# Kernel tuning notes

Hardware: AMD Instinct MI355X
Metric: run time of the kernel (lower is better)

Reference implementation:

```python
import jax, jax.numpy as jnp
import numpy as np

N_NODES = 10000
N_EDGES = 160000
NF = 512  # node_features
DIMS = [1, 2 * NF // 8, 4 * NF // 8, NF]  # 1 -> 128 -> 256 -> 512


def setup_inputs() -> dict:
    key = jax.random.key(0)
    ks = jax.random.split(key, 10)
    inp = {
        "x": jax.random.normal(ks[0], (N_NODES, 1), dtype=jnp.float32),
        "edge_index": jax.random.randint(ks[1], (2, N_EDGES), 0, N_NODES, dtype=jnp.int64),
        "edge_weights": jax.random.uniform(ks[2], (N_EDGES,), dtype=jnp.float32),
    }
    # Glorot-style init for GCNConv linear weights, zero biases (PyG default)
    for i in range(3):
        d_in, d_out = DIMS[i], DIMS[i + 1]
        scale = (6.0 / (d_in + d_out)) ** 0.5
        inp[f"W{i+1}"] = jax.random.uniform(ks[3 + i], (d_in, d_out), dtype=jnp.float32, minval=-scale, maxval=scale)
        inp[f"b{i+1}"] = jnp.zeros((d_out,), dtype=jnp.float32)
    return inp


def _gcn_layer(h, W, b, src, dst, ew):
    # GCNConv with add_self_loops=False, normalize=False:
    #   h' = scatter_sum(edge_weight * (h @ W)[src] -> dst) + b
    h = h @ W                                    # [N, d_out]
    msg = h[src] * ew[:, None]                   # [E, d_out] gather + scale
    agg = jax.ops.segment_sum(msg, dst, num_segments=N_NODES)  # scatter-add
    return agg + b


def reference(x, edge_index, edge_weights, W1, b1, W2, b2, W3, b3):
    src, dst = edge_index[0], edge_index[1]  # source_to_target flow
    h = _gcn_layer(x, W1, b1, src, dst, edge_weights)
    h = _gcn_layer(h, W2, b2, src, dst, edge_weights)
    h = _gcn_layer(h, W3, b3, src, dst, edge_weights)
    return jax.nn.sigmoid(h)
```

## Files before the change

kernel.cpp:

```cpp
#include <hip/hip_runtime.h>
#include <math.h>

#define N_NODES 10000
#define N_EDGES 160000
#define CAP 64


__global__ __launch_bounds__(512) void k0_kernel(
        int* __restrict__ cnt,
        const float* __restrict__ W1, const float* __restrict__ b1,
        const float* __restrict__ W2,
        float* __restrict__ u_part, float* __restrict__ v_part) {
    int tid = threadIdx.x;
    int blk = blockIdx.x;
    if (blk == 0) {
        for (int g = tid; g < N_NODES / 4; g += 512)
            ((int4*)cnt)[g] = make_int4(0, 0, 0, 0);
    } else {
        int b = blk - 1;
        if (tid < 256) {
            int j0 = b * 8;
            float uu = 0.f, vv = 0.f;
            #pragma unroll
            for (int jj = 0; jj < 8; ++jj) {
                float w2 = W2[(j0 + jj) * 256 + tid];
                uu = fmaf(W1[j0 + jj], w2, uu);
                vv = fmaf(b1[j0 + jj], w2, vv);
            }
            u_part[b * 256 + tid] = uu;
            v_part[b * 256 + tid] = vv;
        }
    }
}

__global__ __launch_bounds__(512) void k1_kernel(
        const int* __restrict__ src, const int* __restrict__ dst,
        const float* __restrict__ ew,
        int* __restrict__ cnt, float2* __restrict__ bucket,
        const float* __restrict__ u_part, const float* __restrict__ v_part,
        const float* __restrict__ b2, const float* __restrict__ W3,
        float* __restrict__ p_part, float* __restrict__ q_part,
        float* __restrict__ r_part) {
    int tid = threadIdx.x;
    int blk = blockIdx.x;
    if (blk < 313) {
        int e = blk * 512 + tid;
        if (e < N_EDGES) {
            int   s = src[e];
            int   d = dst[e];
            float w = ew[e];
            int slot = atomicAdd(&cnt[d], 1);
            if (slot < CAP)
                bucket[d * CAP + slot] = make_float2(__int_as_float(s), w);
        }
    } else {
        int c = blk - 313;
        __shared__ float su[16], sv[16], sb[16];
        if (tid < 16) {
            int kk = c * 16 + tid;
            float uu = 0.f, vv = 0.f;
            #pragma unroll
            for (int b = 0; b < 16; ++b) {
                uu += u_part[b * 256 + kk];
                vv += v_part[b * 256 + kk];
            }
            su[tid] = uu; sv[tid] = vv; sb[tid] = b2[kk];
        }
        __syncthreads();
        float pp = 0.f, qq = 0.f, rr = 0.f;
        #pragma unroll
        for (int kk = 0; kk < 16; ++kk) {
            float w3 = W3[(c * 16 + kk) * 512 + tid];
            pp = fmaf(su[kk], w3, pp);
            qq = fmaf(sv[kk], w3, qq);
            rr = fmaf(sb[kk], w3, rr);
        }
        p_part[c * 512 + tid] = pp;
        q_part[c * 512 + tid] = qq;
        r_part[c * 512 + tid] = rr;
    }
}

__global__ __launch_bounds__(512) void k2_kernel(
        const int* __restrict__ cnt, const float2* __restrict__ bucket,
        const float* __restrict__ x, float2* __restrict__ sd,
        const float* __restrict__ p_part, const float* __restrict__ q_part,
        const float* __restrict__ r_part,
        float* __restrict__ p, float* __restrict__ q, float* __restrict__ r) {
    int tid = threadIdx.x;
    int blk = blockIdx.x;
    if (blk < 313) {
        int gid = blk * 512 + tid;
        int n = gid >> 4;
        int l = gid & 15;
        if (n < N_NODES) {
            int c = cnt[n]; if (c > CAP) c = CAP;
            float s1 = 0.f, dg = 0.f;
            for (int i = l; i < c; i += 16) {
                float2 e = bucket[n * CAP + i];
                float w = e.y;
                s1 = fmaf(w, x[__float_as_int(e.x)], s1);
                dg += w;
            }
            #pragma unroll
            for (int m = 1; m < 16; m <<= 1) {
                s1 += __shfl_xor(s1, m);
                dg += __shfl_xor(dg, m);
            }
            if (l == 0) sd[n] = make_float2(s1, dg);
        }
    } else {
        float pp = 0.f, qq = 0.f, rr = 0.f;
        #pragma unroll
        for (int c2 = 0; c2 < 16; ++c2) {
            pp += p_part[c2 * 512 + tid];
            qq += q_part[c2 * 512 + tid];
            rr += r_part[c2 * 512 + tid];
        }
        p[tid] = pp; q[tid] = qq; r[tid] = rr;
    }
}

__global__ __launch_bounds__(512) void k3_kernel(
        const int* __restrict__ cnt, const float2* __restrict__ bucket,
        const float2* __restrict__ sd,
        float* __restrict__ t2, float* __restrict__ Bf) {
    int tid = threadIdx.x;
    int blk = blockIdx.x;
    int gid = blk * 512 + tid;
    int n = gid >> 4;
    int l = gid & 15;
    if (n < N_NODES) {
        int c = cnt[n]; if (c > CAP) c = CAP;
        float tt = 0.f, bb = 0.f;
        for (int i = l; i < c; i += 16) {
            float2 e = bucket[n * CAP + i];
            float2 v = sd[__float_as_int(e.x)];
            tt = fmaf(e.y, v.x, tt);
            bb = fmaf(e.y, v.y, bb);
        }
        #pragma unroll
        for (int m = 1; m < 16; m <<= 1) {
            tt += __shfl_xor(tt, m);
            bb += __shfl_xor(bb, m);
        }
        if (l == 0) { t2[n] = tt; Bf[n] = bb; }
    }
}

__global__ __launch_bounds__(256) void output_kernel(
        const int* __restrict__ cnt, const float2* __restrict__ bucket,
        const float* __restrict__ t2, const float* __restrict__ Bf,
        const float2* __restrict__ sd,
        const float* __restrict__ p, const float* __restrict__ q,
        const float* __restrict__ r, const float* __restrict__ b3,
        float* __restrict__ out) {
    int tid = threadIdx.x;
    int n0 = blockIdx.x * 16;
    __shared__ float A_l[16], B_l[16], D_l[16];
    {
        int nl = tid >> 4;
        int l = tid & 15;
        int n = n0 + nl;
        int c = cnt[n]; if (c > CAP) c = CAP;
        float acc = 0.f;
        for (int i = l; i < c; i += 16) {
            float2 e = bucket[n * CAP + i];
            acc = fmaf(e.y, t2[__float_as_int(e.x)], acc);
        }
        #pragma unroll
        for (int m = 1; m < 16; m <<= 1) acc += __shfl_xor(acc, m);
        if (l == 0) {
            A_l[nl] = acc;
            B_l[nl] = Bf[n];
            D_l[nl] = sd[n].y;
        }
    }
    __syncthreads();
    #pragma unroll
    for (int h = 0; h < 8; ++h) {
        int idx = h * 256 + tid;
        int nl = idx >> 7;
        int j = idx & 127;
        float a = A_l[nl], b = B_l[nl], dg = D_l[nl];
        float4 P = ((const float4*)p)[j];
        float4 Q = ((const float4*)q)[j];
        float4 R = ((const float4*)r)[j];
        float4 B3 = ((const float4*)b3)[j];
        float4 o;
        float zx = fmaf(a, P.x, fmaf(b, Q.x, fmaf(dg, R.x, B3.x)));
        float zy = fmaf(a, P.y, fmaf(b, Q.y, fmaf(dg, R.y, B3.y)));
        float zz = fmaf(a, P.z, fmaf(b, Q.z, fmaf(dg, R.z, B3.z)));
        float zw = fmaf(a, P.w, fmaf(b, Q.w, fmaf(dg, R.w, B3.w)));
        o.x = 1.f / (1.f + __expf(-zx));
        o.y = 1.f / (1.f + __expf(-zy));
        o.z = 1.f / (1.f + __expf(-zz));
        o.w = 1.f / (1.f + __expf(-zw));
        ((float4*)out)[(size_t)(n0 + nl) * 128 + j] = o;
    }
}

extern "C" void kernel_launch(void* const* d_in, const int* in_sizes, int n_in,
                              void* d_out, int out_size, void* d_ws, size_t ws_size,
                              hipStream_t stream) {
    const float* x  = (const float*)d_in[0];
    const int*   ei = (const int*)d_in[1];
    const float* ew = (const float*)d_in[2];
    const float* W1 = (const float*)d_in[3];
    const float* b1 = (const float*)d_in[4];
    const float* W2 = (const float*)d_in[5];
    const float* b2 = (const float*)d_in[6];
    const float* W3 = (const float*)d_in[7];
    const float* b3 = (const float*)d_in[8];
    float* out = (float*)d_out;

    float* ws       = (float*)d_ws;
    int*    cnt     = (int*)ws;
    float2* sd      = (float2*)(ws + 10240);
    float*  t2      = ws + 30240;
    float*  Bf      = ws + 40240;
    float*  p       = ws + 50240;
    float*  q       = ws + 50752;
    float*  r       = ws + 51264;
    float*  u_part  = ws + 51776;
    float*  v_part  = ws + 55872;
    float*  p_part  = ws + 60000;
    float*  q_part  = ws + 68192;
    float*  r_part  = ws + 76384;
    float2* bucket  = (float2*)(ws + 84576);

    const int* src = ei;
    const int* dst = ei + N_EDGES;

    k0_kernel<<<17, 512, 0, stream>>>(cnt, W1, b1, W2, u_part, v_part);
    k1_kernel<<<329, 512, 0, stream>>>(src, dst, ew, cnt, bucket,
                                       u_part, v_part, b2, W3,
                                       p_part, q_part, r_part);
    k2_kernel<<<314, 512, 0, stream>>>(cnt, bucket, x, sd,
                                       p_part, q_part, r_part, p, q, r);
    k3_kernel<<<313, 512, 0, stream>>>(cnt, bucket, sd, t2, Bf);
    output_kernel<<<625, 256, 0, stream>>>(cnt, bucket, t2, Bf, sd,
                                           p, q, r, b3, out);
}
```

Before: 103.5 us.

## Fuse four kernels into persistent mega-kernel with software grid barriers

Merges the bucket-fill, two aggregation stages and the output stage into one persistent kernel of 512 blocks, separated by atomic-counter grid barriers. This removes three kernel launch gaps and their drain/fill tails. In exchange it relies on all 512 blocks being co-resident (launch_bounds 512,4 on a 256-CU part) and adds spin-wait barrier latency. The output stage now loops over tiles with 512 threads, leaving half the threads idle during aggregation.

```diff
diff --git a/kernel.cpp b/kernel.cpp
--- a/kernel.cpp
+++ b/kernel.cpp
@@ -4,10 +4,22 @@
 #define N_NODES 10000
 #define N_EDGES 160000
 #define CAP 64
-
+#define NBLK 512
+
+
+__device__ inline void gbar(int* bar) {
+    __syncthreads();
+    if (threadIdx.x == 0) {
+        __hip_atomic_fetch_add(bar, 1, __ATOMIC_RELEASE, __HIP_MEMORY_SCOPE_AGENT);
+        while (__hip_atomic_load(bar, __ATOMIC_ACQUIRE, __HIP_MEMORY_SCOPE_AGENT) < NBLK) {
+            __builtin_amdgcn_s_sleep(2);
+        }
+    }
+    __syncthreads();
+}
 
 __global__ __launch_bounds__(512) void k0_kernel(
-        int* __restrict__ cnt,
+        int* __restrict__ cnt, int* __restrict__ bar,
         const float* __restrict__ W1, const float* __restrict__ b1,
         const float* __restrict__ W2,
         float* __restrict__ u_part, float* __restrict__ v_part) {
@@ -16,6 +28,7 @@
     if (blk == 0) {
         for (int g = tid; g < N_NODES / 4; g += 512)
             ((int4*)cnt)[g] = make_int4(0, 0, 0, 0);
+        if (tid < 16) bar[tid] = 0;
     } else {
         int b = blk - 1;
         if (tid < 256) {
@@ -33,16 +46,23 @@
     }
 }
 
-__global__ __launch_bounds__(512) void k1_kernel(
+__global__ __launch_bounds__(512, 4) void mega_kernel(
         const int* __restrict__ src, const int* __restrict__ dst,
-        const float* __restrict__ ew,
-        int* __restrict__ cnt, float2* __restrict__ bucket,
+        const float* __restrict__ ew, const float* __restrict__ x,
+        int* __restrict__ cnt, int* __restrict__ bar,
+        float2* __restrict__ bucket, float2* __restrict__ sd,
+        float* __restrict__ t2, float* __restrict__ Bf,
         const float* __restrict__ u_part, const float* __restrict__ v_part,
         const float* __restrict__ b2, const float* __restrict__ W3,
         float* __restrict__ p_part, float* __restrict__ q_part,
-        float* __restrict__ r_part) {
+        float* __restrict__ r_part,
+        float* __restrict__ p, float* __restrict__ q, float* __restrict__ r,
+        const float* __restrict__ b3, float* __restrict__ out) {
     int tid = threadIdx.x;
     int blk = blockIdx.x;
+    __shared__ float su[16], sv[16], sb[16];
+    __shared__ float A_l[16], B_l[16], D_l[16];
+
     if (blk < 313) {
         int e = blk * 512 + tid;
         if (e < N_EDGES) {
@@ -53,9 +73,8 @@
             if (slot < CAP)
                 bucket[d * CAP + slot] = make_float2(__int_as_float(s), w);
         }
-    } else {
+    } else if (blk < 329) {
         int c = blk - 313;
-        __shared__ float su[16], sv[16], sb[16];
         if (tid < 16) {
             int kk = c * 16 + tid;
             float uu = 0.f, vv = 0.f;
@@ -79,16 +98,8 @@
         q_part[c * 512 + tid] = qq;
         r_part[c * 512 + tid] = rr;
     }
-}
-
-__global__ __launch_bounds__(512) void k2_kernel(
-        const int* __restrict__ cnt, const float2* __restrict__ bucket,
-        const float* __restrict__ x, float2* __restrict__ sd,
-        const float* __restrict__ p_part, const float* __restrict__ q_part,
-        const float* __restrict__ r_part,
-        float* __restrict__ p, float* __restrict__ q, float* __restrict__ r) {
-    int tid = threadIdx.x;
-    int blk = blockIdx.x;
+    gbar(&bar[0]);
+
     if (blk < 313) {
         int gid = blk * 512 + tid;
         int n = gid >> 4;
@@ -98,9 +109,8 @@
             float s1 = 0.f, dg = 0.f;
             for (int i = l; i < c; i += 16) {
                 float2 e = bucket[n * CAP + i];
-                float w = e.y;
-                s1 = fmaf(w, x[__float_as_int(e.x)], s1);
-                dg += w;
+                s1 = fmaf(e.y, x[__float_as_int(e.x)], s1);
+                dg += e.y;
             }
             #pragma unroll
             for (int m = 1; m < 16; m <<= 1) {
@@ -109,7 +119,30 @@
             }
             if (l == 0) sd[n] = make_float2(s1, dg);
         }
-    } else {
+    }
+    gbar(&bar[1]);
+
+    if (blk < 313) {
+        int gid = blk * 512 + tid;
+        int n = gid >> 4;
+        int l = gid & 15;
+        if (n < N_NODES) {
+            int c = cnt[n]; if (c > CAP) c = CAP;
+            float tt = 0.f, bb = 0.f;
+            for (int i = l; i < c; i += 16) {
+                float2 e = bucket[n * CAP + i];
+                float2 v = sd[__float_as_int(e.x)];
+                tt = fmaf(e.y, v.x, tt);
+                bb = fmaf(e.y, v.y, bb);
+            }
+            #pragma unroll
+            for (int m = 1; m < 16; m <<= 1) {
+                tt += __shfl_xor(tt, m);
+                bb += __shfl_xor(bb, m);
+            }
+            if (l == 0) { t2[n] = tt; Bf[n] = bb; }
+        }
+    } else if (blk == 400) {
         float pp = 0.f, qq = 0.f, rr = 0.f;
         #pragma unroll
         for (int c2 = 0; c2 < 16; ++c2) {
@@ -119,84 +152,51 @@
         }
         p[tid] = pp; q[tid] = qq; r[tid] = rr;
     }
-}
-
-__global__ __launch_bounds__(512) void k3_kernel(
-        const int* __restrict__ cnt, const float2* __restrict__ bucket,
-        const float2* __restrict__ sd,
-        float* __restrict__ t2, float* __restrict__ Bf) {
-    int tid = threadIdx.x;
-    int blk = blockIdx.x;
-    int gid = blk * 512 + tid;
-    int n = gid >> 4;
-    int l = gid & 15;
-    if (n < N_NODES) {
-        int c = cnt[n]; if (c > CAP) c = CAP;
-        float tt = 0.f, bb = 0.f;
-        for (int i = l; i < c; i += 16) {
-            float2 e = bucket[n * CAP + i];
-            float2 v = sd[__float_as_int(e.x)];
-            tt = fmaf(e.y, v.x, tt);
-            bb = fmaf(e.y, v.y, bb);
-        }
+    gbar(&bar[2]);
+
+    for (int t = blk; t < 625; t += NBLK) {
+        int n0 = t * 16;
+        if (tid < 256) {
+            int nl = tid >> 4;
+            int l = tid & 15;
+            int n = n0 + nl;
+            int c = cnt[n]; if (c > CAP) c = CAP;
+            float acc = 0.f;
+            for (int i = l; i < c; i += 16) {
+                float2 e = bucket[n * CAP + i];
+                acc = fmaf(e.y, t2[__float_as_int(e.x)], acc);
+            }
+            #pragma unroll
+            for (int m = 1; m < 16; m <<= 1) acc += __shfl_xor(acc, m);
+            if (l == 0) {
+                A_l[nl] = acc;
+                B_l[nl] = Bf[n];
+                D_l[nl] = sd[n].y;
+            }
+        }
+        __syncthreads();
         #pragma unroll
-        for (int m = 1; m < 16; m <<= 1) {
-            tt += __shfl_xor(tt, m);
-            bb += __shfl_xor(bb, m);
-        }
-        if (l == 0) { t2[n] = tt; Bf[n] = bb; }
-    }
-}
-
-__global__ __launch_bounds__(256) void output_kernel(
-        const int* __restrict__ cnt, const float2* __restrict__ bucket,
-        const float* __restrict__ t2, const float* __restrict__ Bf,
-        const float2* __restrict__ sd,
-        const float* __restrict__ p, const float* __restrict__ q,
-        const float* __restrict__ r, const float* __restrict__ b3,
-        float* __restrict__ out) {
-    int tid = threadIdx.x;
-    int n0 = blockIdx.x * 16;
-    __shared__ float A_l[16], B_l[16], D_l[16];
-    {
-        int nl = tid >> 4;
-        int l = tid & 15;
-        int n = n0 + nl;
-        int c = cnt[n]; if (c > CAP) c = CAP;
-        float acc = 0.f;
-        for (int i = l; i < c; i += 16) {
-            float2 e = bucket[n * CAP + i];
-            acc = fmaf(e.y, t2[__float_as_int(e.x)], acc);
-        }
-        #pragma unroll
-        for (int m = 1; m < 16; m <<= 1) acc += __shfl_xor(acc, m);
-        if (l == 0) {
-            A_l[nl] = acc;
-            B_l[nl] = Bf[n];
-            D_l[nl] = sd[n].y;
-        }
-    }
-    __syncthreads();
-    #pragma unroll
-    for (int h = 0; h < 8; ++h) {
-        int idx = h * 256 + tid;
-        int nl = idx >> 7;
-        int j = idx & 127;
-        float a = A_l[nl], b = B_l[nl], dg = D_l[nl];
-        float4 P = ((const float4*)p)[j];
-        float4 Q = ((const float4*)q)[j];
-        float4 R = ((const float4*)r)[j];
-        float4 B3 = ((const float4*)b3)[j];
-        float4 o;
-        float zx = fmaf(a, P.x, fmaf(b, Q.x, fmaf(dg, R.x, B3.x)));
-        float zy = fmaf(a, P.y, fmaf(b, Q.y, fmaf(dg, R.y, B3.y)));
-        float zz = fmaf(a, P.z, fmaf(b, Q.z, fmaf(dg, R.z, B3.z)));
-        float zw = fmaf(a, P.w, fmaf(b, Q.w, fmaf(dg, R.w, B3.w)));
-        o.x = 1.f / (1.f + __expf(-zx));
-        o.y = 1.f / (1.f + __expf(-zy));
-        o.z = 1.f / (1.f + __expf(-zz));
-        o.w = 1.f / (1.f + __expf(-zw));
-        ((float4*)out)[(size_t)(n0 + nl) * 128 + j] = o;
+        for (int h = 0; h < 4; ++h) {
+            int idx = h * 512 + tid;
+            int nl = idx >> 7;
+            int j = idx & 127;
+            float a = A_l[nl], b = B_l[nl], dg = D_l[nl];
+            float4 P = ((const float4*)p)[j];
+            float4 Q = ((const float4*)q)[j];
+            float4 R = ((const float4*)r)[j];
+            float4 B3 = ((const float4*)b3)[j];
+            float4 o;
+            float zx = fmaf(a, P.x, fmaf(b, Q.x, fmaf(dg, R.x, B3.x)));
+            float zy = fmaf(a, P.y, fmaf(b, Q.y, fmaf(dg, R.y, B3.y)));
+            float zz = fmaf(a, P.z, fmaf(b, Q.z, fmaf(dg, R.z, B3.z)));
+            float zw = fmaf(a, P.w, fmaf(b, Q.w, fmaf(dg, R.w, B3.w)));
+            o.x = 1.f / (1.f + __expf(-zx));
+            o.y = 1.f / (1.f + __expf(-zy));
+            o.z = 1.f / (1.f + __expf(-zz));
+            o.w = 1.f / (1.f + __expf(-zw));
+            ((float4*)out)[(size_t)(n0 + nl) * 128 + j] = o;
+        }
+        __syncthreads();
     }
 }
 
@@ -216,29 +216,27 @@
 
     float* ws       = (float*)d_ws;
     int*    cnt     = (int*)ws;
-    float2* sd      = (float2*)(ws + 10240);
-    float*  t2      = ws + 30240;
-    float*  Bf      = ws + 40240;
-    float*  p       = ws + 50240;
-    float*  q       = ws + 50752;
-    float*  r       = ws + 51264;
-    float*  u_part  = ws + 51776;
-    float*  v_part  = ws + 55872;
-    float*  p_part  = ws + 60000;
-    float*  q_part  = ws + 68192;
-    float*  r_part  = ws + 76384;
-    float2* bucket  = (float2*)(ws + 84576);
+    int*    bar     = (int*)(ws + 10240);
+    float2* sd      = (float2*)(ws + 10752);
+    float*  t2      = ws + 30752;
+    float*  Bf      = ws + 40752;
+    float*  p       = ws + 50752;
+    float*  q       = ws + 51264;
+    float*  r       = ws + 51776;
+    float*  u_part  = ws + 52288;
+    float*  v_part  = ws + 56384;
+    float*  p_part  = ws + 60480;
+    float*  q_part  = ws + 68672;
+    float*  r_part  = ws + 76864;
+    float2* bucket  = (float2*)(ws + 85056);
 
     const int* src = ei;
     const int* dst = ei + N_EDGES;
 
-    k0_kernel<<<17, 512, 0, stream>>>(cnt, W1, b1, W2, u_part, v_part);
-    k1_kernel<<<329, 512, 0, stream>>>(src, dst, ew, cnt, bucket,
-                                       u_part, v_part, b2, W3,
-                                       p_part, q_part, r_part);
-    k2_kernel<<<314, 512, 0, stream>>>(cnt, bucket, x, sd,
-                                       p_part, q_part, r_part, p, q, r);
-    k3_kernel<<<313, 512, 0, stream>>>(cnt, bucket, sd, t2, Bf);
-    output_kernel<<<625, 256, 0, stream>>>(cnt, bucket, t2, Bf, sd,
-                                           p, q, r, b3, out);
-}
+    k0_kernel<<<17, 512, 0, stream>>>(cnt, bar, W1, b1, W2, u_part, v_part);
+    mega_kernel<<<NBLK, 512, 0, stream>>>(src, dst, ew, x, cnt, bar,
+                                          bucket, sd, t2, Bf,
+                                          u_part, v_part, b2, W3,
+                                          p_part, q_part, r_part, p, q, r,
+                                          b3, out);
+}
```

Result: slower. 268.5 us (+159.4%).
